# Optimization experiments

Hardware: AMD Instinct MI355X
Metric: run time of the kernel (lower is better)

The kernel has to match this reference:

```python
import jax, jax.numpy as jnp
import numpy as np

N_ENT = 200000   # n_entities
N_NODES = 20000  # nodes in subgraph
N_EDGES = 320000 # avg degree 16
R = 40           # n_relations
B = 34           # num_bases (hard-coded in module)
D_IN = 128       # emb_dim_init
D_HID = 128      # hidden_dim
D_OUT = 128      # out_dim


def setup_inputs() -> dict:
    key = jax.random.key(0)
    ks = jax.random.split(key, 14)
    s = 0.05
    return {
        "node_index": jax.random.randint(ks[0], (N_NODES,), 0, N_ENT),
        "edge_index": jax.random.randint(ks[1], (2, N_EDGES), 0, N_NODES),
        "edge_type": jax.random.randint(ks[2], (N_EDGES,), 0, R),
        "node_frequency": jax.random.normal(ks[3], (N_NODES,), jnp.float32),
        "node_emb": jax.random.normal(ks[4], (N_ENT, D_IN), jnp.float32),
        "comp0": jax.random.normal(ks[5], (R, B), jnp.float32) * s,
        "bases0": jax.random.normal(ks[6], (B, D_IN, D_HID), jnp.float32) * s,
        "root0": jax.random.normal(ks[7], (D_IN, D_HID), jnp.float32) * s,
        "bias0": jnp.zeros((D_HID,), jnp.float32),
        "comp1": jax.random.normal(ks[8], (R, B), jnp.float32) * s,
        "bases1": jax.random.normal(ks[9], (B, D_HID, D_OUT), jnp.float32) * s,
        "root1": jax.random.normal(ks[10], (D_HID, D_OUT), jnp.float32) * s,
        "bias1": jnp.zeros((D_OUT,), jnp.float32),
    }


def _rgcn_conv(x, src, dst, etype, comp, bases, root, bias):
    """Basis-decomposed RGCNConv (PyG semantics: per-relation mean aggregation
    over incoming edges, plus root transform and bias)."""
    n = x.shape[0]
    # relation weights from basis decomposition: [R, in, out]
    W = jnp.einsum('rb,bio->rio', comp, bases)
    # transform all nodes by every relation weight: [R, N, out]
    h_all = jnp.einsum('ni,rio->rno', x, W)
    # gather per-edge message x[src] @ W[edge_type]: [E, out]
    msg = h_all[etype, src]
    # mean-aggregate per (dst node, relation) segment
    seg = dst * R + etype
    sums = jax.ops.segment_sum(msg, seg, num_segments=n * R)  # [N*R, out]
    cnt = jax.ops.segment_sum(jnp.ones((msg.shape[0],), x.dtype), seg,
                              num_segments=n * R)
    mean = sums / jnp.maximum(cnt, 1.0)[:, None]
    agg = mean.reshape(n, R, -1).sum(axis=1)  # sum over relations: [N, out]
    return agg + x @ root + bias


def reference(node_index, edge_index, edge_type, node_frequency, node_emb,
              comp0, bases0, root0, bias0, comp1, bases1, root1, bias1):
    # node_frequency is accepted but unused (matches original forward).
    x = node_emb[node_index]                      # [N, D_IN]
    src, dst = edge_index[0], edge_index[1]
    x = _rgcn_conv(x, src, dst, edge_type, comp0, bases0, root0, bias0)
    x = _rgcn_conv(x, src, dst, edge_type, comp1, bases1, root1, bias1)
    return x
```

## Files before the change

### kernel.cpp

```cpp
#include <hip/hip_runtime.h>

#define N_NODES  20000
#define N_EDGES  320000
#define R_REL    40
#define N_BASES  34
#define DIM      128
#define EB       128
#define P_PAD    (N_EDGES + R_REL * EB)
#define ROOT_PAD ((N_NODES + EB - 1) / EB * EB)
#define P2_MAX   (P_PAD + ROOT_PAD)
#define NE2      (N_EDGES + N_NODES)
#define NSLOT    (R_REL + 1)

typedef unsigned int uint;
typedef unsigned short ushort;
typedef __attribute__((ext_vector_type(8))) short short8;
typedef __attribute__((ext_vector_type(4))) float f32x4;

__device__ __forceinline__ ushort f2bf(float f) {
    uint u = __float_as_uint(f);
    return (ushort)((u + 0x7FFFu + ((u >> 16) & 1u)) >> 16);
}
__device__ __forceinline__ uint pk2bf(float a, float b) {
    return (uint)f2bf(a) | ((uint)f2bf(b) << 16);
}

__global__ void init_kernel(int* __restrict__ c_cnt, int* __restrict__ meta_cur2_deg,
                            uint4* __restrict__ esrc) {
    int i = blockIdx.x * blockDim.x + threadIdx.x;
    if (i < N_NODES * R_REL) c_cnt[i] = 0;
    if (i < P2_MAX) esrc[i] = make_uint4((uint)-1, (uint)-1, 0u, 0u);
    if (i < 256 + 2 * N_NODES) meta_cur2_deg[i] = 0;
}

__global__ void count_kernel(const int* __restrict__ ei, const int* __restrict__ et,
                             int* __restrict__ c, int* __restrict__ h,
                             int* __restrict__ deg) {
    __shared__ int hloc[R_REL];
    int t = threadIdx.x;
    if (t < R_REL) hloc[t] = 0;
    __syncthreads();
    int e = blockIdx.x * blockDim.x + t;
    if (e < N_EDGES) {
        int dst = ei[N_EDGES + e];
        int r   = et[e];
        atomicAdd(&c[dst * R_REL + r], 1);
        atomicAdd(&deg[dst], 1);
        atomicAdd(&hloc[r], 1);
    }
    __syncthreads();
    if (t < R_REL && hloc[t]) atomicAdd(&h[t], hloc[t]);
}

__global__ void scans_kernel(const int* __restrict__ deg, const int* __restrict__ h,
                             int* __restrict__ ptr, int* __restrict__ off) {
    __shared__ int part[1024];
    const int CHn = (N_NODES + 1023) / 1024;
    int t = threadIdx.x;
    int s = 0;
    for (int i = 0; i < CHn; ++i) {
        int idx = t * CHn + i;
        if (idx < N_NODES) s += deg[idx] + 1;
    }
    part[t] = s;
    __syncthreads();
    for (int d = 1; d < 1024; d <<= 1) {
        int v = (t >= d) ? part[t - d] : 0;
        __syncthreads();
        part[t] += v;
        __syncthreads();
    }
    int base = (t > 0) ? part[t - 1] : 0;
    for (int i = 0; i < CHn; ++i) {
        int idx = t * CHn + i;
        if (idx < N_NODES) { ptr[idx] = base; base += deg[idx] + 1; }
    }
    if (t == 0) {
        ptr[N_NODES] = NE2;
        int acc = 0;
        off[0] = 0;
        for (int r = 0; r < R_REL; ++r) {
            acc += ((h[r] + EB - 1) / EB) * EB;
            off[r + 1] = acc;
        }
        off[R_REL + 1] = acc + ROOT_PAD;
    }
}

__global__ void place_kernel(const int* __restrict__ ei, const int* __restrict__ et,
                             const int* __restrict__ off, int* __restrict__ cur,
                             const int* __restrict__ c_cnt,
                             const int* __restrict__ ptr, int* __restrict__ cur2,
                             uint4* __restrict__ esrc) {
    __shared__ int hloc[R_REL];
    __shared__ int base[R_REL];
    int t = threadIdx.x;
    if (t < R_REL) hloc[t] = 0;
    __syncthreads();
    int e = blockIdx.x * blockDim.x + t;
    int r = 0, myrank = 0, src = 0, dst = 0;
    bool isEdge = (e < N_EDGES);
    if (isEdge) {
        r = et[e]; src = ei[e]; dst = ei[N_EDGES + e];
        myrank = atomicAdd(&hloc[r], 1);
    }
    __syncthreads();
    if (t < R_REL) base[t] = hloc[t] ? atomicAdd(&cur[t], hloc[t]) : 0;
    __syncthreads();
    if (isEdge) {
        int p = off[r] + base[r] + myrank;
        int q = ptr[dst] + 1 + atomicAdd(&cur2[dst], 1);
        int cnt = c_cnt[dst * R_REL + r];
        float esc = 1.0f / (float)(cnt < 1 ? 1 : cnt);
        esrc[p] = make_uint4((uint)src, (uint)q, __float_as_uint(esc), 0u);
    } else if (e < N_EDGES + N_NODES) {
        int n = e - N_EDGES;
        esrc[off[R_REL] + n] = make_uint4((uint)n, (uint)ptr[n], 0x3f800000u, 0u);
    }
}

__global__ void gather_bf16_kernel(const float* __restrict__ emb, const int* __restrict__ idx,
                                   ushort* __restrict__ xb) {
    int t = blockIdx.x * blockDim.x + threadIdx.x;
    int n = t >> 4, v = t & 15;
    const float4* s = (const float4*)(emb + (size_t)idx[n] * DIM + v * 8);
    float4 a = s[0], b = s[1];
    uint4 o;
    o.x = pk2bf(a.x, a.y); o.y = pk2bf(a.z, a.w);
    o.z = pk2bf(b.x, b.y); o.w = pk2bf(b.z, b.w);
    *(uint4*)(xb + (size_t)n * DIM + v * 8) = o;
}

__global__ void wtrans_kernel(const float* __restrict__ comp0, const float* __restrict__ bases0,
                              const float* __restrict__ root0,
                              const float* __restrict__ comp1, const float* __restrict__ bases1,
                              const float* __restrict__ root1,
                              ushort* __restrict__ Wt) {
    __shared__ float tile[32][33];
    __shared__ float scomp[N_BASES];
    int b = blockIdx.x;
    int layer = (b >= NSLOT * 16) ? 1 : 0;
    int bb = b - layer * NSLOT * 16;
    const float* comp  = layer ? comp1  : comp0;
    const float* bases = layer ? bases1 : bases0;
    const float* root  = layer ? root1  : root0;
    int slot = bb >> 4;
    int tb   = bb & 15;
    int k0 = (tb >> 2) * 32, n0 = (tb & 3) * 32;
    int t = threadIdx.x, tr = t >> 5, tc = t & 31;
    if (slot < R_REL) {
        if (t < N_BASES) scomp[t] = comp[slot * N_BASES + t];
        __syncthreads();
        #pragma unroll
        for (int i = 0; i < 4; ++i) {
            int kk = tr + 8 * i;
            float acc = 0.f;
            #pragma unroll
            for (int bs = 0; bs < N_BASES; ++bs)
                acc += scomp[bs] * bases[((size_t)bs * DIM + k0 + kk) * DIM + n0 + tc];
            tile[kk][tc] = acc;
        }
    } else {
        #pragma unroll
        for (int i = 0; i < 4; ++i) {
            int kk = tr + 8 * i;
            tile[kk][tc] = root[(size_t)(k0 + kk) * DIM + n0 + tc];
        }
    }
    __syncthreads();
    size_t obase = ((size_t)layer * NSLOT + slot) * DIM * DIM;
    #pragma unroll
    for (int i = 0; i < 4; ++i) {
        int rr = tr + 8 * i;
        Wt[obase + (size_t)(n0 + rr) * DIM + k0 + tc] = f2bf(tile[tc][rr]);
    }
}

__launch_bounds__(256)
__global__ void edge_mfma_kernel(const uint4* __restrict__ esrc, const int* __restrict__ off,
                                 const ushort* __restrict__ xb, const ushort* __restrict__ Wt,
                                 ushort* __restrict__ T) {
    __shared__ __align__(16) ushort Ws[DIM * DIM];
    __shared__ int soff[R_REL + 2];
    int t = threadIdx.x;
    int e0 = blockIdx.x * EB;
    int wv = t >> 6;
    int l  = t & 63;
    int lr = l & 15;
    int lk = l >> 4;
    int er0 = e0 + wv * 32 + lr;
    int er1 = er0 + 16;
    uint4 es0 = esrc[er0], es1 = esrc[er1];

    if (t < R_REL + 2) soff[t] = off[t];
    __syncthreads();
    if (e0 >= soff[R_REL + 1]) return;
    int r = 0;
    while (e0 >= soff[r + 1]) ++r;

    const ushort* Wr = Wt + (size_t)r * DIM * DIM;
    #pragma unroll
    for (int i = 0; i < 8; ++i) {
        int idx = t + 256 * i;
        int row = idx >> 4, slot = idx & 15;
        uint4 v = *(const uint4*)(Wr + row * DIM + slot * 8);
        *(uint4*)(&Ws[row * DIM + ((slot ^ (row & 15)) * 8)]) = v;
    }

    int s0 = (int)es0.x, q0 = (int)es0.y;
    int s1 = (int)es1.x, q1 = (int)es1.y;
    float esc0 = __uint_as_float(es0.z), esc1 = __uint_as_float(es1.z);
    const ushort* x0p = xb + (size_t)(s0 < 0 ? 0 : s0) * DIM;
    const ushort* x1p = xb + (size_t)(s1 < 0 ? 0 : s1) * DIM;
    short8 xf0[4], xf1[4];
    #pragma unroll
    for (int ks = 0; ks < 4; ++ks) {
        xf0[ks] = *(const short8*)(x0p + (ks * 4 + lk) * 8);
        xf1[ks] = *(const short8*)(x1p + (ks * 4 + lk) * 8);
    }
    __syncthreads();

    f32x4 acc0[8], acc1[8];
    #pragma unroll
    for (int mt = 0; mt < 8; ++mt) {
        acc0[mt] = (f32x4){0.f, 0.f, 0.f, 0.f};
        acc1[mt] = (f32x4){0.f, 0.f, 0.f, 0.f};
    }

    #pragma unroll
    for (int ks = 0; ks < 4; ++ks) {
        #pragma unroll
        for (int mt = 0; mt < 8; ++mt) {
            int row = mt * 16 + lr;
            int slot = (ks * 4 + lk) ^ lr;
            short8 wf = *(const short8*)(&Ws[row * DIM + slot * 8]);
            acc0[mt] = __builtin_amdgcn_mfma_f32_16x16x32_bf16(wf, xf0[ks], acc0[mt], 0, 0, 0);
            acc1[mt] = __builtin_amdgcn_mfma_f32_16x16x32_bf16(wf, xf1[ks], acc1[mt], 0, 0, 0);
        }
    }

    ushort* T0 = T + (size_t)q0 * DIM;
    ushort* T1 = T + (size_t)q1 * DIM;
    #pragma unroll
    for (int mt = 0; mt < 8; ++mt) {
        if (q0 >= 0) {
            uint2 p0;
            p0.x = pk2bf(acc0[mt][0] * esc0, acc0[mt][1] * esc0);
            p0.y = pk2bf(acc0[mt][2] * esc0, acc0[mt][3] * esc0);
            *(uint2*)(T0 + mt * 16 + lk * 4) = p0;
        }
        if (q1 >= 0) {
            uint2 p1;
            p1.x = pk2bf(acc1[mt][0] * esc1, acc1[mt][1] * esc1);
            p1.y = pk2bf(acc1[mt][2] * esc1, acc1[mt][3] * esc1);
            *(uint2*)(T1 + mt * 16 + lk * 4) = p1;
        }
    }
}

template<int OUT_BF16>
__global__ void aggregate_kernel(const int* __restrict__ ptr, const ushort* __restrict__ T,
                                 const float* __restrict__ bias, void* __restrict__ yout) {
    int t = threadIdx.x;
    int n = blockIdx.x * 2 + (t >> 6);
    int tt = t & 63;
    int s0 = ptr[n], s1 = ptr[n + 1];
    float a0 = bias[2 * tt], a1 = bias[2 * tt + 1];
    for (int q = s0; q < s1; ++q) {
        uint v = *(const uint*)(T + (size_t)q * DIM + 2 * tt);
        a0 += __uint_as_float(v << 16);
        a1 += __uint_as_float(v & 0xFFFF0000u);
    }
    if (OUT_BF16) {
        ((uint*)yout)[n * 64 + tt] = pk2bf(a0, a1);
    } else {
        ((float2*)yout)[n * 64 + tt] = make_float2(a0, a1);
    }
}

extern "C" void kernel_launch(void* const* d_in, const int* in_sizes, int n_in,
                              void* d_out, int out_size, void* d_ws, size_t ws_size,
                              hipStream_t stream) {
    const int*   node_index = (const int*)d_in[0];
    const int*   edge_index = (const int*)d_in[1];
    const int*   edge_type  = (const int*)d_in[2];
    const float* node_emb   = (const float*)d_in[4];
    const float* comp0  = (const float*)d_in[5];
    const float* bases0 = (const float*)d_in[6];
    const float* root0  = (const float*)d_in[7];
    const float* bias0  = (const float*)d_in[8];
    const float* comp1  = (const float*)d_in[9];
    const float* bases1 = (const float*)d_in[10];
    const float* root1  = (const float*)d_in[11];
    const float* bias1  = (const float*)d_in[12];
    float* out = (float*)d_out;

    char* ws = (char*)d_ws;
    int*    c_cnt  = (int*)   (ws);
    ushort* Wt     = (ushort*)(ws +  3200000);
    ushort* x0b    = (ushort*)(ws +  5886976);
    ushort* y0b    = (ushort*)(ws + 11006976);
    uint4*  esrc   = (uint4*) (ws + 16126976);
    int*    meta   = (int*)   (ws + 21650432);
    int*    cur2   = (int*)   (ws + 21651456);
    int*    deg    = (int*)   (ws + 21731456);
    int*    ptr    = (int*)   (ws + 21811456);
    ushort* T      = (ushort*)(ws + 21891712);
    int* off = meta;
    int* h   = meta + 64;
    int* cur = meta + 128;

    init_kernel<<<(N_NODES * R_REL + 255) / 256, 256, 0, stream>>>(c_cnt, meta, esrc);
    count_kernel<<<(N_EDGES + 255) / 256, 256, 0, stream>>>(edge_index, edge_type, c_cnt, h, deg);
    scans_kernel<<<1, 1024, 0, stream>>>(deg, h, ptr, off);
    place_kernel<<<(N_EDGES + N_NODES + 255) / 256, 256, 0, stream>>>(
        edge_index, edge_type, off, cur, c_cnt, ptr, cur2, esrc);
    gather_bf16_kernel<<<N_NODES * 16 / 256, 256, 0, stream>>>(node_emb, node_index, x0b);
    wtrans_kernel<<<2 * NSLOT * 16, 256, 0, stream>>>(comp0, bases0, root0,
                                                      comp1, bases1, root1, Wt);

    const int eBlocks = P2_MAX / EB;

    edge_mfma_kernel<<<eBlocks, 256, 0, stream>>>(esrc, off, x0b, Wt, T);
    aggregate_kernel<1><<<N_NODES / 2, 128, 0, stream>>>(ptr, T, bias0, y0b);

    edge_mfma_kernel<<<eBlocks, 256, 0, stream>>>(esrc, off, y0b,
                                                  Wt + (size_t)NSLOT * DIM * DIM, T);
    aggregate_kernel<0><<<N_NODES / 2, 128, 0, stream>>>(ptr, T, bias1, out);
}
```

Before: 274.0 us.

## Merge prep kernels into one launch and use 512-thread edge blocks

After: 256.4 us. 6.4% less time.

```diff
diff --git a/kernel.cpp b/kernel.cpp
--- a/kernel.cpp
+++ b/kernel.cpp
@@ -12,6 +12,10 @@
 #define NE2      (N_EDGES + N_NODES)
 #define NSLOT    (R_REL + 1)
 
+#define INIT_B   ((N_NODES * R_REL + 255) / 256)
+#define GATH_B   (N_NODES * 16 / 256)
+#define WT_B     (2 * NSLOT * 16)
+
 typedef unsigned int uint;
 typedef unsigned short ushort;
 typedef __attribute__((ext_vector_type(8))) short short8;
@@ -25,12 +29,71 @@
     return (uint)f2bf(a) | ((uint)f2bf(b) << 16);
 }
 
-__global__ void init_kernel(int* __restrict__ c_cnt, int* __restrict__ meta_cur2_deg,
-                            uint4* __restrict__ esrc) {
-    int i = blockIdx.x * blockDim.x + threadIdx.x;
-    if (i < N_NODES * R_REL) c_cnt[i] = 0;
-    if (i < P2_MAX) esrc[i] = make_uint4((uint)-1, (uint)-1, 0u, 0u);
-    if (i < 256 + 2 * N_NODES) meta_cur2_deg[i] = 0;
+__global__ void prep_kernel(int* __restrict__ c_cnt, int* __restrict__ meta_cur2_deg,
+                            uint4* __restrict__ esrc,
+                            const float* __restrict__ emb, const int* __restrict__ idx,
+                            ushort* __restrict__ xb,
+                            const float* __restrict__ comp0, const float* __restrict__ bases0,
+                            const float* __restrict__ root0,
+                            const float* __restrict__ comp1, const float* __restrict__ bases1,
+                            const float* __restrict__ root1,
+                            ushort* __restrict__ Wt) {
+    int b = blockIdx.x;
+    int t = threadIdx.x;
+    if (b < INIT_B) {
+        int i = b * 256 + t;
+        if (i < N_NODES * R_REL) c_cnt[i] = 0;
+        if (i < P2_MAX) esrc[i] = make_uint4((uint)-1, (uint)-1, 0u, 0u);
+        if (i < 256 + 2 * N_NODES) meta_cur2_deg[i] = 0;
+    } else if (b < INIT_B + GATH_B) {
+        int g = (b - INIT_B) * 256 + t;
+        int n = g >> 4, v = g & 15;
+        const float4* s = (const float4*)(emb + (size_t)idx[n] * DIM + v * 8);
+        float4 a = s[0], bb = s[1];
+        uint4 o;
+        o.x = pk2bf(a.x, a.y);  o.y = pk2bf(a.z, a.w);
+        o.z = pk2bf(bb.x, bb.y); o.w = pk2bf(bb.z, bb.w);
+        *(uint4*)(xb + (size_t)n * DIM + v * 8) = o;
+    } else {
+        __shared__ float tile[32][33];
+        __shared__ float scomp[N_BASES];
+        int wb = b - INIT_B - GATH_B;
+        int layer = (wb >= NSLOT * 16) ? 1 : 0;
+        int bb2 = wb - layer * NSLOT * 16;
+        const float* comp  = layer ? comp1  : comp0;
+        const float* bases = layer ? bases1 : bases0;
+        const float* root  = layer ? root1  : root0;
+        int slot = bb2 >> 4;
+        int tb   = bb2 & 15;
+        int k0 = (tb >> 2) * 32, n0 = (tb & 3) * 32;
+        int tr = t >> 5, tc = t & 31;
+        if (slot < R_REL) {
+            if (t < N_BASES) scomp[t] = comp[slot * N_BASES + t];
+            __syncthreads();
+            #pragma unroll
+            for (int i = 0; i < 4; ++i) {
+                int kk = tr + 8 * i;
+                float acc = 0.f;
+                #pragma unroll
+                for (int bs = 0; bs < N_BASES; ++bs)
+                    acc += scomp[bs] * bases[((size_t)bs * DIM + k0 + kk) * DIM + n0 + tc];
+                tile[kk][tc] = acc;
+            }
+        } else {
+            #pragma unroll
+            for (int i = 0; i < 4; ++i) {
+                int kk = tr + 8 * i;
+                tile[kk][tc] = root[(size_t)(k0 + kk) * DIM + n0 + tc];
+            }
+        }
+        __syncthreads();
+        size_t obase = ((size_t)layer * NSLOT + slot) * DIM * DIM;
+        #pragma unroll
+        for (int i = 0; i < 4; ++i) {
+            int rr = tr + 8 * i;
+            Wt[obase + (size_t)(n0 + rr) * DIM + k0 + tc] = f2bf(tile[tc][rr]);
+        }
+    }
 }
 
 __global__ void count_kernel(const int* __restrict__ ei, const int* __restrict__ et,
@@ -119,64 +182,7 @@
     }
 }
 
-__global__ void gather_bf16_kernel(const float* __restrict__ emb, const int* __restrict__ idx,
-                                   ushort* __restrict__ xb) {
-    int t = blockIdx.x * blockDim.x + threadIdx.x;
-    int n = t >> 4, v = t & 15;
-    const float4* s = (const float4*)(emb + (size_t)idx[n] * DIM + v * 8);
-    float4 a = s[0], b = s[1];
-    uint4 o;
-    o.x = pk2bf(a.x, a.y); o.y = pk2bf(a.z, a.w);
-    o.z = pk2bf(b.x, b.y); o.w = pk2bf(b.z, b.w);
-    *(uint4*)(xb + (size_t)n * DIM + v * 8) = o;
-}
-
-__global__ void wtrans_kernel(const float* __restrict__ comp0, const float* __restrict__ bases0,
-                              const float* __restrict__ root0,
-                              const float* __restrict__ comp1, const float* __restrict__ bases1,
-                              const float* __restrict__ root1,
-                              ushort* __restrict__ Wt) {
-    __shared__ float tile[32][33];
-    __shared__ float scomp[N_BASES];
-    int b = blockIdx.x;
-    int layer = (b >= NSLOT * 16) ? 1 : 0;
-    int bb = b - layer * NSLOT * 16;
-    const float* comp  = layer ? comp1  : comp0;
-    const float* bases = layer ? bases1 : bases0;
-    const float* root  = layer ? root1  : root0;
-    int slot = bb >> 4;
-    int tb   = bb & 15;
-    int k0 = (tb >> 2) * 32, n0 = (tb & 3) * 32;
-    int t = threadIdx.x, tr = t >> 5, tc = t & 31;
-    if (slot < R_REL) {
-        if (t < N_BASES) scomp[t] = comp[slot * N_BASES + t];
-        __syncthreads();
-        #pragma unroll
-        for (int i = 0; i < 4; ++i) {
-            int kk = tr + 8 * i;
-            float acc = 0.f;
-            #pragma unroll
-            for (int bs = 0; bs < N_BASES; ++bs)
-                acc += scomp[bs] * bases[((size_t)bs * DIM + k0 + kk) * DIM + n0 + tc];
-            tile[kk][tc] = acc;
-        }
-    } else {
-        #pragma unroll
-        for (int i = 0; i < 4; ++i) {
-            int kk = tr + 8 * i;
-            tile[kk][tc] = root[(size_t)(k0 + kk) * DIM + n0 + tc];
-        }
-    }
-    __syncthreads();
-    size_t obase = ((size_t)layer * NSLOT + slot) * DIM * DIM;
-    #pragma unroll
-    for (int i = 0; i < 4; ++i) {
-        int rr = tr + 8 * i;
-        Wt[obase + (size_t)(n0 + rr) * DIM + k0 + tc] = f2bf(tile[tc][rr]);
-    }
-}
-
-__launch_bounds__(256)
+__launch_bounds__(512)
 __global__ void edge_mfma_kernel(const uint4* __restrict__ esrc, const int* __restrict__ off,
                                  const ushort* __restrict__ xb, const ushort* __restrict__ Wt,
                                  ushort* __restrict__ T) {
@@ -188,9 +194,8 @@
     int l  = t & 63;
     int lr = l & 15;
     int lk = l >> 4;
-    int er0 = e0 + wv * 32 + lr;
-    int er1 = er0 + 16;
-    uint4 es0 = esrc[er0], es1 = esrc[er1];
+    int er = e0 + wv * 16 + lr;
+    uint4 es = esrc[er];
 
     if (t < R_REL + 2) soff[t] = off[t];
     __syncthreads();
@@ -200,32 +205,25 @@
 
     const ushort* Wr = Wt + (size_t)r * DIM * DIM;
     #pragma unroll
-    for (int i = 0; i < 8; ++i) {
-        int idx = t + 256 * i;
+    for (int i = 0; i < 4; ++i) {
+        int idx = t + 512 * i;
         int row = idx >> 4, slot = idx & 15;
         uint4 v = *(const uint4*)(Wr + row * DIM + slot * 8);
         *(uint4*)(&Ws[row * DIM + ((slot ^ (row & 15)) * 8)]) = v;
     }
 
-    int s0 = (int)es0.x, q0 = (int)es0.y;
-    int s1 = (int)es1.x, q1 = (int)es1.y;
-    float esc0 = __uint_as_float(es0.z), esc1 = __uint_as_float(es1.z);
-    const ushort* x0p = xb + (size_t)(s0 < 0 ? 0 : s0) * DIM;
-    const ushort* x1p = xb + (size_t)(s1 < 0 ? 0 : s1) * DIM;
-    short8 xf0[4], xf1[4];
+    int s0 = (int)es.x, q0 = (int)es.y;
+    float esc = __uint_as_float(es.z);
+    const ushort* xp = xb + (size_t)(s0 < 0 ? 0 : s0) * DIM;
+    short8 xf[4];
     #pragma unroll
-    for (int ks = 0; ks < 4; ++ks) {
-        xf0[ks] = *(const short8*)(x0p + (ks * 4 + lk) * 8);
-        xf1[ks] = *(const short8*)(x1p + (ks * 4 + lk) * 8);
-    }
-    __syncthreads();
-
-    f32x4 acc0[8], acc1[8];
+    for (int ks = 0; ks < 4; ++ks)
+        xf[ks] = *(const short8*)(xp + (ks * 4 + lk) * 8);
+    __syncthreads();
+
+    f32x4 acc[8];
     #pragma unroll
-    for (int mt = 0; mt < 8; ++mt) {
-        acc0[mt] = (f32x4){0.f, 0.f, 0.f, 0.f};
-        acc1[mt] = (f32x4){0.f, 0.f, 0.f, 0.f};
-    }
+    for (int mt = 0; mt < 8; ++mt) acc[mt] = (f32x4){0.f, 0.f, 0.f, 0.f};
 
     #pragma unroll
     for (int ks = 0; ks < 4; ++ks) {
@@ -234,26 +232,18 @@
             int row = mt * 16 + lr;
             int slot = (ks * 4 + lk) ^ lr;
             short8 wf = *(const short8*)(&Ws[row * DIM + slot * 8]);
-            acc0[mt] = __builtin_amdgcn_mfma_f32_16x16x32_bf16(wf, xf0[ks], acc0[mt], 0, 0, 0);
-            acc1[mt] = __builtin_amdgcn_mfma_f32_16x16x32_bf16(wf, xf1[ks], acc1[mt], 0, 0, 0);
-        }
-    }
-
-    ushort* T0 = T + (size_t)q0 * DIM;
-    ushort* T1 = T + (size_t)q1 * DIM;
-    #pragma unroll
-    for (int mt = 0; mt < 8; ++mt) {
-        if (q0 >= 0) {
+            acc[mt] = __builtin_amdgcn_mfma_f32_16x16x32_bf16(wf, xf[ks], acc[mt], 0, 0, 0);
+        }
+    }
+
+    if (q0 >= 0) {
+        ushort* T0 = T + (size_t)q0 * DIM;
+        #pragma unroll
+        for (int mt = 0; mt < 8; ++mt) {
             uint2 p0;
-            p0.x = pk2bf(acc0[mt][0] * esc0, acc0[mt][1] * esc0);
-            p0.y = pk2bf(acc0[mt][2] * esc0, acc0[mt][3] * esc0);
+            p0.x = pk2bf(acc[mt][0] * esc, acc[mt][1] * esc);
+            p0.y = pk2bf(acc[mt][2] * esc, acc[mt][3] * esc);
             *(uint2*)(T0 + mt * 16 + lk * 4) = p0;
-        }
-        if (q1 >= 0) {
-            uint2 p1;
-            p1.x = pk2bf(acc1[mt][0] * esc1, acc1[mt][1] * esc1);
-            p1.y = pk2bf(acc1[mt][2] * esc1, acc1[mt][3] * esc1);
-            *(uint2*)(T1 + mt * 16 + lk * 4) = p1;
         }
     }
 }
@@ -310,21 +300,20 @@
     int* h   = meta + 64;
     int* cur = meta + 128;
 
-    init_kernel<<<(N_NODES * R_REL + 255) / 256, 256, 0, stream>>>(c_cnt, meta, esrc);
+    prep_kernel<<<INIT_B + GATH_B + WT_B, 256, 0, stream>>>(
+        c_cnt, meta, esrc, node_emb, node_index, x0b,
+        comp0, bases0, root0, comp1, bases1, root1, Wt);
     count_kernel<<<(N_EDGES + 255) / 256, 256, 0, stream>>>(edge_index, edge_type, c_cnt, h, deg);
     scans_kernel<<<1, 1024, 0, stream>>>(deg, h, ptr, off);
     place_kernel<<<(N_EDGES + N_NODES + 255) / 256, 256, 0, stream>>>(
         edge_index, edge_type, off, cur, c_cnt, ptr, cur2, esrc);
-    gather_bf16_kernel<<<N_NODES * 16 / 256, 256, 0, stream>>>(node_emb, node_index, x0b);
-    wtrans_kernel<<<2 * NSLOT * 16, 256, 0, stream>>>(comp0, bases0, root0,
-                                                      comp1, bases1, root1, Wt);
 
     const int eBlocks = P2_MAX / EB;
 
-    edge_mfma_kernel<<<eBlocks, 256, 0, stream>>>(esrc, off, x0b, Wt, T);
+    edge_mfma_kernel<<<eBlocks, 512, 0, stream>>>(esrc, off, x0b, Wt, T);
     aggregate_kernel<1><<<N_NODES / 2, 128, 0, stream>>>(ptr, T, bias0, y0b);
 
-    edge_mfma_kernel<<<eBlocks, 256, 0, stream>>>(esrc, off, y0b,
+    edge_mfma_kernel<<<eBlocks, 512, 0, stream>>>(esrc, off, y0b,
                                                   Wt + (size_t)NSLOT * DIM * DIM, T);
     aggregate_kernel<0><<<N_NODES / 2, 128, 0, stream>>>(ptr, T, bias1, out);
 }
```
